# Optimization experiments

Measured on AMD Instinct MI355X. Metric: run time of the kernel, lower is better.

Reference implementation:

```python
import jax, jax.numpy as jnp
import numpy as np

N = 2048      # factor dims (d_in == units == N)
K = 16        # nonzeros per row of each factor
B = 16384     # batch
F = 3         # number of sparse factors
NNZ = N * K


def _pattern(f):
    # Fixed, compile-time-known structured sparsity pattern (butterfly-like):
    # row r has nonzeros at cols (r + k*(N//K) + f) % N, k in [0, K)
    r = np.repeat(np.arange(N), K)
    k = np.tile(np.arange(K), N)
    c = (r + k * (N // K) + f) % N
    return r.astype(np.int32), c.astype(np.int32)


def setup_inputs() -> dict:
    key = jax.random.key(0)
    kx, k0, k1, k2, ks, kb = jax.random.split(key, 6)
    # glorot-ish scale for sparse factor values: fan ~ K nonzeros per row
    wscale = (2.0 / (K + K)) ** 0.5
    rows0, cols0 = _pattern(0)
    rows1, cols1 = _pattern(1)
    rows2, cols2 = _pattern(2)
    return {
        "x": jax.random.normal(kx, (B, N), dtype=jnp.float32),
        "vals0": jax.random.normal(k0, (NNZ,), dtype=jnp.float32) * wscale,
        "vals1": jax.random.normal(k1, (NNZ,), dtype=jnp.float32) * wscale,
        "vals2": jax.random.normal(k2, (NNZ,), dtype=jnp.float32) * wscale,
        "rows0": jnp.asarray(rows0), "cols0": jnp.asarray(cols0),
        "rows1": jnp.asarray(rows1), "cols1": jnp.asarray(cols1),
        "rows2": jnp.asarray(rows2), "cols2": jnp.asarray(cols2),
        "scaling": jax.random.uniform(ks, (1,), dtype=jnp.float32, minval=0.5, maxval=1.5),
        "bias": jax.random.normal(kb, (N,), dtype=jnp.float32) * 0.02,
    }


def _dense_factor(vals, rows, cols):
    # materialize the sparse factor (values scattered into the fixed pattern)
    return jnp.zeros((N, N), dtype=vals.dtype).at[rows, cols].set(vals)


def reference(x, vals0, vals1, vals2, rows0, cols0, rows1, cols1, rows2, cols2, scaling, bias):
    # output = relu(scaling * (x @ W0 @ W1 @ W2) + bias)
    y = x
    for vals, rows, cols in ((vals0, rows0, cols0), (vals1, rows1, cols1), (vals2, rows2, cols2)):
        y = y @ _dense_factor(vals, rows, cols)  # [B, N]
    y = scaling * y + bias
    return jax.nn.relu(y)
```

## Files before the change

kernel.cpp:

```cpp
#include <hip/hip_runtime.h>

#define NN 2048
#define KK 16

__global__ __launch_bounds__(256) void sfd_compose01(const float* __restrict__ v0,
                                                     const float* __restrict__ v1,
                                                     float* __restrict__ w01) {
  int tid = blockIdx.x * 256 + threadIdx.x;
  int c1 = tid >> 4;
  int i  = tid & 15;
  int cm = (c1 + NN - 1) & (NN - 1);
  int s1 = cm & 127;
  int t1 = cm >> 7;
  int rx = s1 + (i << 7);
  float acc = 0.f;
#pragma unroll
  for (int k1 = 0; k1 < 16; ++k1) {
    int r0 = (cm - (k1 << 7)) & (NN - 1);
    int k0 = (t1 - k1 - i) & 15;
    acc = fmaf(v1[r0 * 16 + k1], v0[rx * 16 + k0], acc);
  }
  w01[c1 * 16 + i] = acc;
}

__global__ __launch_bounds__(256) void sfd_compose012(const float* __restrict__ v2,
                                                      const float* __restrict__ w01,
                                                      const float* __restrict__ scaling,
                                                      float* __restrict__ mcl) {
  int tid = blockIdx.x * 256 + threadIdx.x;
  int c = tid >> 4;
  int i = tid & 15;
  float acc = 0.f;
#pragma unroll
  for (int k2 = 0; k2 < 16; ++k2) {
    int r1 = (c + NN - 2 - (k2 << 7)) & (NN - 1);
    acc = fmaf(v2[r1 * 16 + k2], w01[r1 * 16 + i], acc);
  }
  int s = c & 127;
  int j = c >> 7;
  mcl[(s * 16 + j) * 16 + i] = acc * scaling[0];
}

__device__ __forceinline__ void sfd_loadq(float4 (&pf)[4], const float* __restrict__ x,
                                          int rb, int w0, int t) {
#pragma unroll
  for (int q = 0; q < 4; ++q) {
    int idx = t + (q << 8);
    int uu = idx & 31;
    int ig = (idx >> 5) & 3;
    int rr = idx >> 7;
    const float* xrow = x + (size_t)(rb + rr) * NN;
    int cb = w0 + uu + (ig << 9);
    pf[q].x = xrow[cb & (NN - 1)];
    pf[q].y = xrow[(cb + 128) & (NN - 1)];
    pf[q].z = xrow[(cb + 256) & (NN - 1)];
    pf[q].w = xrow[(cb + 384) & (NN - 1)];
  }
}

__device__ __forceinline__ void sfd_writeq(const float4 (&pf)[4], float* xs, int t) {
#pragma unroll
  for (int q = 0; q < 4; ++q) {
    int idx = t + (q << 8);
    int uu = idx & 31;
    int ig = (idx >> 5) & 3;
    int rr = idx >> 7;
    *(float4*)(xs + (rr * 32 + uu) * 20 + (ig << 2)) = pf[q];
  }
}

__device__ __forceinline__ void sfd_compute(const float* xs, int u,
                                            const float (&mc0)[16], const float (&mc1)[16],
                                            float bi0, float bi1,
                                            int rb, int c0, int c1,
                                            float* __restrict__ out) {
#pragma unroll 1
  for (int r = 0; r < 8; ++r) {
    const float4* xr = (const float4*)(xs + (r * 32 + u) * 20);
    float xv[16];
    *(float4*)(xv + 0)  = xr[0];
    *(float4*)(xv + 4)  = xr[1];
    *(float4*)(xv + 8)  = xr[2];
    *(float4*)(xv + 12) = xr[3];
    float acc0 = bi0, acc1 = bi1;
#pragma unroll
    for (int i = 0; i < 16; ++i) {
      acc0 = fmaf(xv[i], mc0[i], acc0);
      acc1 = fmaf(xv[i], mc1[i], acc1);
    }
    size_t ob = (size_t)(rb + r) * NN;
    __builtin_nontemporal_store(fmaxf(acc0, 0.f), &out[ob + c0]);
    __builtin_nontemporal_store(fmaxf(acc1, 0.f), &out[ob + c1]);
  }
}

__global__ __launch_bounds__(256, 4) void sfd_apply(const float* __restrict__ x,
                                                    const float* __restrict__ mcl,
                                                    const float* __restrict__ bias,
                                                    float* __restrict__ out) {
  const int S0 = blockIdx.x << 5;
  const int b0 = blockIdx.y << 5;
  const int t = threadIdx.x;
  const int u = t & 31;
  const int jp = t >> 5;
  const int s = S0 + u;
  const int j0 = jp << 1;
  const int w0 = (S0 + 125) & 127;
  const int shift = (w0 + u) >> 7;

  float mc0[16], mc1[16];
  {
    const float* r0p = mcl + ((s * 16 + j0) << 4);
#pragma unroll
    for (int i = 0; i < 16; ++i) {
      int ic = (i + shift) & 15;
      mc0[i] = r0p[ic];
      mc1[i] = r0p[16 + ic];
    }
  }
  const int c0 = s + (j0 << 7);
  const int c1 = c0 + 128;
  const float bi0 = bias[c0];
  const float bi1 = bias[c1];

  __shared__ float xs[8 * 32 * 20];

  float4 pfA[4], pfB[4];

  sfd_loadq(pfA, x, b0 + 0,  w0, t);
  sfd_writeq(pfA, xs, t);
  sfd_loadq(pfB, x, b0 + 8,  w0, t);
  __syncthreads();
  sfd_compute(xs, u, mc0, mc1, bi0, bi1, b0 + 0,  c0, c1, out);
  __syncthreads();
  sfd_writeq(pfB, xs, t);
  sfd_loadq(pfA, x, b0 + 16, w0, t);
  __syncthreads();
  sfd_compute(xs, u, mc0, mc1, bi0, bi1, b0 + 8,  c0, c1, out);
  __syncthreads();
  sfd_writeq(pfA, xs, t);
  sfd_loadq(pfB, x, b0 + 24, w0, t);
  __syncthreads();
  sfd_compute(xs, u, mc0, mc1, bi0, bi1, b0 + 16, c0, c1, out);
  __syncthreads();
  sfd_writeq(pfB, xs, t);
  __syncthreads();
  sfd_compute(xs, u, mc0, mc1, bi0, bi1, b0 + 24, c0, c1, out);
}

extern "C" void kernel_launch(void* const* d_in, const int* in_sizes, int n_in,
                              void* d_out, int out_size, void* d_ws, size_t ws_size,
                              hipStream_t stream) {
  const float* x       = (const float*)d_in[0];
  const float* v0      = (const float*)d_in[1];
  const float* v1      = (const float*)d_in[2];
  const float* v2      = (const float*)d_in[3];
  const float* scaling = (const float*)d_in[10];
  const float* bias    = (const float*)d_in[11];
  float* out = (float*)d_out;

  float* w01 = (float*)d_ws;
  float* mcl = w01 + NN * KK;

  const int B = in_sizes[0] / NN;

  hipLaunchKernelGGL(sfd_compose01, dim3(128), dim3(256), 0, stream, v0, v1, w01);
  hipLaunchKernelGGL(sfd_compose012, dim3(128), dim3(256), 0, stream, v2, w01, scaling, mcl);
  hipLaunchKernelGGL(sfd_apply, dim3(4, B >> 5), dim3(256), 0, stream, x, mcl, bias, out);
}
```

Baseline: 265.7 us.

## Fuse factor-composition kernels and double-buffer shared tile in apply kernel

Merges the two small kernels that compose the three sparse factors into one, recomputing the intermediate W0·W1 entries in registers instead of writing them to a workspace, which removes one kernel launch and a global round trip. The apply kernel gets a double-buffered shared-memory tile, so each compute step no longer needs a trailing barrier before the next tile is written. The fused compose recomputes the inner products redundantly (16x more FMAs) and doubles the LDS use of the apply kernel, which may lower occupancy.

```diff
diff --git a/kernel.cpp b/kernel.cpp
--- a/kernel.cpp
+++ b/kernel.cpp
@@ -3,38 +3,37 @@
 #define NN 2048
 #define KK 16
 
-__global__ __launch_bounds__(256) void sfd_compose01(const float* __restrict__ v0,
-                                                     const float* __restrict__ v1,
-                                                     float* __restrict__ w01) {
-  int tid = blockIdx.x * 256 + threadIdx.x;
-  int c1 = tid >> 4;
-  int i  = tid & 15;
-  int cm = (c1 + NN - 1) & (NN - 1);
-  int s1 = cm & 127;
-  int t1 = cm >> 7;
-  int rx = s1 + (i << 7);
-  float acc = 0.f;
-#pragma unroll
-  for (int k1 = 0; k1 < 16; ++k1) {
-    int r0 = (cm - (k1 << 7)) & (NN - 1);
-    int k0 = (t1 - k1 - i) & 15;
-    acc = fmaf(v1[r0 * 16 + k1], v0[rx * 16 + k0], acc);
-  }
-  w01[c1 * 16 + i] = acc;
-}
-
-__global__ __launch_bounds__(256) void sfd_compose012(const float* __restrict__ v2,
-                                                      const float* __restrict__ w01,
-                                                      const float* __restrict__ scaling,
-                                                      float* __restrict__ mcl) {
-  int tid = blockIdx.x * 256 + threadIdx.x;
+__global__ __launch_bounds__(128) void sfd_compose(const float* __restrict__ v0,
+                                                   const float* __restrict__ v1,
+                                                   const float* __restrict__ v2,
+                                                   const float* __restrict__ scaling,
+                                                   float* __restrict__ mcl) {
+  int tid = blockIdx.x * 128 + threadIdx.x;
   int c = tid >> 4;
   int i = tid & 15;
+
+  int A  = (c + NN - 3) & (NN - 1);
+  int s1 = A & 127;
+  int T0 = A >> 7;
+  int rx = s1 + (i << 7);
+
+  float vr[16];
+#pragma unroll
+  for (int m = 0; m < 16; ++m)
+    vr[m] = v0[rx * 16 + ((T0 - i - m) & 15)];
+
   float acc = 0.f;
-#pragma unroll
+#pragma unroll 4
   for (int k2 = 0; k2 < 16; ++k2) {
     int r1 = (c + NN - 2 - (k2 << 7)) & (NN - 1);
-    acc = fmaf(v2[r1 * 16 + k2], w01[r1 * 16 + i], acc);
+    int cm = (r1 + NN - 1) & (NN - 1);
+    float w = 0.f;
+#pragma unroll
+    for (int k1 = 0; k1 < 16; ++k1) {
+      int r0 = (cm - (k1 << 7)) & (NN - 1);
+      w = fmaf(v1[r0 * 16 + k1], vr[(k1 + k2) & 15], w);
+    }
+    acc = fmaf(v2[r1 * 16 + k2], w, acc);
   }
   int s = c & 127;
   int j = c >> 7;
@@ -123,29 +122,30 @@
   const float bi0 = bias[c0];
   const float bi1 = bias[c1];
 
-  __shared__ float xs[8 * 32 * 20];
+  __shared__ float xs[2][8 * 32 * 20];
 
   float4 pfA[4], pfB[4];
 
   sfd_loadq(pfA, x, b0 + 0,  w0, t);
-  sfd_writeq(pfA, xs, t);
+  sfd_writeq(pfA, xs[0], t);
   sfd_loadq(pfB, x, b0 + 8,  w0, t);
   __syncthreads();
-  sfd_compute(xs, u, mc0, mc1, bi0, bi1, b0 + 0,  c0, c1, out);
-  __syncthreads();
-  sfd_writeq(pfB, xs, t);
+
+  sfd_compute(xs[0], u, mc0, mc1, bi0, bi1, b0 + 0,  c0, c1, out);
+  sfd_writeq(pfB, xs[1], t);
   sfd_loadq(pfA, x, b0 + 16, w0, t);
   __syncthreads();
-  sfd_compute(xs, u, mc0, mc1, bi0, bi1, b0 + 8,  c0, c1, out);
-  __syncthreads();
-  sfd_writeq(pfA, xs, t);
+
+  sfd_compute(xs[1], u, mc0, mc1, bi0, bi1, b0 + 8,  c0, c1, out);
+  sfd_writeq(pfA, xs[0], t);
   sfd_loadq(pfB, x, b0 + 24, w0, t);
   __syncthreads();
-  sfd_compute(xs, u, mc0, mc1, bi0, bi1, b0 + 16, c0, c1, out);
+
+  sfd_compute(xs[0], u, mc0, mc1, bi0, bi1, b0 + 16, c0, c1, out);
+  sfd_writeq(pfB, xs[1], t);
   __syncthreads();
-  sfd_writeq(pfB, xs, t);
-  __syncthreads();
-  sfd_compute(xs, u, mc0, mc1, bi0, bi1, b0 + 24, c0, c1, out);
+
+  sfd_compute(xs[1], u, mc0, mc1, bi0, bi1, b0 + 24, c0, c1, out);
 }
 
 extern "C" void kernel_launch(void* const* d_in, const int* in_sizes, int n_in,
@@ -159,12 +159,10 @@
   const float* bias    = (const float*)d_in[11];
   float* out = (float*)d_out;
 
-  float* w01 = (float*)d_ws;
-  float* mcl = w01 + NN * KK;
+  float* mcl = (float*)d_ws;
 
   const int B = in_sizes[0] / NN;
 
-  hipLaunchKernelGGL(sfd_compose01, dim3(128), dim3(256), 0, stream, v0, v1, w01);
-  hipLaunchKernelGGL(sfd_compose012, dim3(128), dim3(256), 0, stream, v2, w01, scaling, mcl);
+  hipLaunchKernelGGL(sfd_compose, dim3(256), dim3(128), 0, stream, v0, v1, v2, scaling, mcl);
   hipLaunchKernelGGL(sfd_apply, dim3(4, B >> 5), dim3(256), 0, stream, x, mcl, bias, out);
 }
```

Measured after the change: 268.2 us. Within noise of the previous version (+1.0%).
